# Kernel optimization log

Hardware: AMD Instinct MI355X
Metric: run time of the kernel (lower is better)

Reference implementation:

```python
import jax, jax.numpy as jnp
import numpy as np

N = 16384      # points
C = 512        # channels (d_model)
D_INNER = 1024 # expand=2
D_STATE = 16
D_CONV = 4
DT_RANK = 32   # ceil(C/16)
MLP = 1024     # mlp_ratio=2
EPS = 1e-5


def setup_inputs() -> dict:
    key = jax.random.key(0)
    ks = jax.random.split(key, 16)
    s = 0.02
    feat = jax.random.normal(ks[0], (N, C), jnp.float32)
    perm = np.random.RandomState(0).permutation(N)
    order = jnp.asarray(perm, jnp.int32)
    inverse = jnp.asarray(np.argsort(perm), jnp.int32)
    inp = dict(
        feat=feat, order=order, inverse=inverse,
        ln1_w=jnp.ones((C,)), ln1_b=jnp.zeros((C,)),
        in_proj_w=s * jax.random.normal(ks[1], (2 * D_INNER, C)),
        conv_w=s * jax.random.normal(ks[2], (D_INNER, D_CONV)),
        conv_b=jnp.zeros((D_INNER,)),
        x_proj_w=s * jax.random.normal(ks[3], (DT_RANK + 2 * D_STATE, D_INNER)),
        dt_proj_w=s * jax.random.normal(ks[4], (D_INNER, DT_RANK)),
        dt_proj_b=jnp.full((D_INNER,), -2.0),  # softplus(-2) ~ small dt, like mamba init
        A_log=jnp.log(jnp.tile(jnp.arange(1, D_STATE + 1, dtype=jnp.float32)[None, :], (D_INNER, 1))),
        D_skip=jnp.ones((D_INNER,)),
        out_proj_w=s * jax.random.normal(ks[5], (C, D_INNER)),
        ln2_w=jnp.ones((C,)), ln2_b=jnp.zeros((C,)),
        ffn_w1=s * jax.random.normal(ks[6], (C, MLP)), ffn_b1=jnp.zeros((MLP,)),
        ffn_w2=s * jax.random.normal(ks[7], (MLP, C)), ffn_b2=jnp.zeros((C,)),
    )
    return inp


def _layer_norm(x, w, b):
    mu = jnp.mean(x, axis=-1, keepdims=True)
    var = jnp.mean(jnp.square(x - mu), axis=-1, keepdims=True)
    return (x - mu) * jax.lax.rsqrt(var + EPS) * w + b


def _mamba(x, in_proj_w, conv_w, conv_b, x_proj_w, dt_proj_w, dt_proj_b,
           A_log, D_skip, out_proj_w):
    # x: (L, C)
    L = x.shape[0]
    xz = x @ in_proj_w.T                      # (L, 2*D_INNER)
    xm, z = jnp.split(xz, 2, axis=-1)
    # depthwise causal conv1d, kernel D_CONV
    xp = jnp.pad(xm, ((D_CONV - 1, 0), (0, 0)))
    xc = conv_b + sum(xp[k:k + L] * conv_w[:, k] for k in range(D_CONV))
    xc = jax.nn.silu(xc)                      # (L, D_INNER)
    dbc = xc @ x_proj_w.T                     # (L, DT_RANK + 2*D_STATE)
    dt, Bm, Cm = jnp.split(dbc, [DT_RANK, DT_RANK + D_STATE], axis=-1)
    dt = jax.nn.softplus(dt @ dt_proj_w.T + dt_proj_b)  # (L, D_INNER)
    A = -jnp.exp(A_log)                       # (D_INNER, D_STATE)

    def step(h, inp):
        dt_t, B_t, C_t, x_t = inp             # (D_INNER,), (D_STATE,), (D_STATE,), (D_INNER,)
        dA = jnp.exp(dt_t[:, None] * A)       # (D_INNER, D_STATE)
        h = dA * h + (dt_t * x_t)[:, None] * B_t[None, :]
        return h, h @ C_t                     # y_t: (D_INNER,)

    h0 = jnp.zeros((D_INNER, D_STATE), xm.dtype)
    _, ys = jax.lax.scan(step, h0, (dt, Bm, Cm, xc))
    y = (ys + xc * D_skip) * jax.nn.silu(z)
    return y @ out_proj_w.T                   # (L, C)


def reference(feat, order, inverse, ln1_w, ln1_b, in_proj_w, conv_w, conv_b,
              x_proj_w, dt_proj_w, dt_proj_b, A_log, D_skip, out_proj_w,
              ln2_w, ln2_b, ffn_w1, ffn_b1, ffn_w2, ffn_b2):
    f = feat[order]                           # gather by serialized order
    x = f + _mamba(_layer_norm(f, ln1_w, ln1_b), in_proj_w, conv_w, conv_b,
                   x_proj_w, dt_proj_w, dt_proj_b, A_log, D_skip, out_proj_w)
    h = _layer_norm(x, ln2_w, ln2_b)
    x = x + (jax.nn.gelu(h @ ffn_w1 + ffn_b1, approximate=False) @ ffn_w2 + ffn_b2)
    return x[inverse]                         # scatter back to original order
```

## Files before the change

kernel.cpp:

```cpp
#include <hip/hip_runtime.h>


#define DEV __device__ __forceinline__

typedef unsigned short u16;
typedef u16    u16x8  __attribute__((ext_vector_type(8)));
typedef __bf16 bf16x8 __attribute__((ext_vector_type(8)));
typedef float  f32x4  __attribute__((ext_vector_type(4)));

static constexpr int L_SEQ = 16384;
static constexpr int LC    = 64;
static constexpr int NCH   = 256;

DEV u16 f2b(float x){
  union { float f; unsigned u; } c; c.f = x;
  unsigned u = c.u;
  return (u16)((u + 0x7fffu + ((u >> 16) & 1u)) >> 16);
}
DEV float b2f(u16 h){
  union { unsigned u; float f; } c; c.u = ((unsigned)h) << 16;
  return c.f;
}
DEV int ldix(const void* p, int l, bool is64){
  return is64 ? (int)((const long long*)p)[l] : ((const int*)p)[l];
}
DEV float siluf(float x){ return x / (1.f + __expf(-x)); }
DEV float softplusf(float x){
  return fmaxf(x, 0.f) + __logf(1.f + __expf(-fabsf(x)));
}
DEV float geluf(float x){ return 0.5f * x * (1.f + erff(x * 0.70710678118f)); }

DEV void gld_lds16(const u16* g, u16* l){
  __builtin_amdgcn_global_load_lds(
      (const __attribute__((address_space(1))) unsigned*)g,
      (__attribute__((address_space(3))) unsigned*)l, 16, 0, 0);
}

DEV void pow16(float r, float* a){
  float r2 = r * r, r4 = r2 * r2, r8 = r4 * r4;
  a[0] = r;        a[1] = r2;       a[2] = r2 * r;    a[3] = r4;
  a[4] = r4 * r;   a[5] = r4 * r2;  a[6] = r4 * a[2]; a[7] = r8;
  a[8] = r8 * r;   a[9] = r8 * r2;  a[10] = r8 * a[2]; a[11] = r8 * r4;
  a[12] = r8 * a[4]; a[13] = r8 * a[5]; a[14] = r8 * a[6]; a[15] = r8 * r8;
}

__global__ __launch_bounds__(256) void fill_k(float* out, float v, unsigned n){
  unsigned i = blockIdx.x * 256 + threadIdx.x;
  if (i < n) out[i] = v;
}

__global__ void detect_k(const int* ord32, int* flag){
  flag[0] = (ord32[1] == 0 && ord32[3] == 0 && ord32[5] == 0) ? 1 : 0;
  flag[1] = 0;
}

__global__ __launch_bounds__(256) void checkA_k(const float* __restrict__ alog,
                                                int* flag){
  int i = blockIdx.x * 256 + threadIdx.x;
  int s = i & 15;
  float v = alog[i];
  float base = alog[i - s];
  if (fabsf(v - (base + __logf((float)(s + 1)))) > 1e-4f) atomicOr(flag + 1, 1);
}

struct NT4 { const float* src[4]; unsigned off[5]; };
__global__ __launch_bounds__(256) void normw_k(NT4 t, u16* dst){
  unsigned i = blockIdx.x * 256 + threadIdx.x;
  if (i >= t.off[4]) return;
  int s = 0;
  #pragma unroll
  for (int k = 1; k <= 3; k++) s += (i >= t.off[k]) ? 1 : 0;
  dst[i] = f2b(t.src[s][i - t.off[s]]);
}

__global__ __launch_bounds__(256) void convT_kernel(const float* __restrict__ in,
                                                    u16* __restrict__ out, int K, int N){
  __shared__ float t[32][33];
  int k0 = blockIdx.x * 32, n0 = blockIdx.y * 32;
  int tx = threadIdx.x & 31, ty = threadIdx.x >> 5;
  #pragma unroll
  for (int i = 0; i < 32; i += 8)
    t[ty + i][tx] = in[(size_t)(k0 + ty + i) * N + n0 + tx];
  __syncthreads();
  #pragma unroll
  for (int i = 0; i < 32; i += 8)
    out[(size_t)(n0 + ty + i) * K + k0 + tx] = f2b(t[tx][ty + i]);
}

__global__ __launch_bounds__(256) void gather_ln1(const float* __restrict__ feat,
    const void* order, const float* __restrict__ w, const float* __restrict__ b,
    const int* flag, u16* __restrict__ x1b){
  __shared__ float rs_[256], rq_[256];
  const bool is64 = flag[0] != 0;
  int l = blockIdx.x, tid = threadIdx.x;
  int src = ldix(order, l, is64);
  float v0 = feat[(size_t)src * 512 + tid];
  float v1 = feat[(size_t)src * 512 + tid + 256];
  rs_[tid] = v0 + v1; rq_[tid] = v0 * v0 + v1 * v1;
  __syncthreads();
  for (int o = 128; o; o >>= 1){
    if (tid < o){ rs_[tid] += rs_[tid + o]; rq_[tid] += rq_[tid + o]; }
    __syncthreads();
  }
  float mu = rs_[0] * (1.f / 512.f);
  float var = rq_[0] * (1.f / 512.f) - mu * mu;
  float rstd = rsqrtf(var + 1e-5f);
  x1b[(size_t)l * 512 + tid]       = f2b((v0 - mu) * rstd * w[tid]       + b[tid]);
  x1b[(size_t)l * 512 + tid + 256] = f2b((v1 - mu) * rstd * w[tid + 256] + b[tid + 256]);
}

__global__ __launch_bounds__(256) void ln2_kernel(const float* __restrict__ x,
    const float* __restrict__ w, const float* __restrict__ b, u16* __restrict__ h2b){
  __shared__ float rs_[256], rq_[256];
  int l = blockIdx.x, tid = threadIdx.x;
  float v0 = x[(size_t)l * 512 + tid];
  float v1 = x[(size_t)l * 512 + tid + 256];
  rs_[tid] = v0 + v1; rq_[tid] = v0 * v0 + v1 * v1;
  __syncthreads();
  for (int o = 128; o; o >>= 1){
    if (tid < o){ rs_[tid] += rs_[tid + o]; rq_[tid] += rq_[tid + o]; }
    __syncthreads();
  }
  float mu = rs_[0] * (1.f / 512.f);
  float var = rq_[0] * (1.f / 512.f) - mu * mu;
  float rstd = rsqrtf(var + 1e-5f);
  h2b[(size_t)l * 512 + tid]       = f2b((v0 - mu) * rstd * w[tid]       + b[tid]);
  h2b[(size_t)l * 512 + tid + 256] = f2b((v1 - mu) * rstd * w[tid + 256] + b[tid + 256]);
}

__global__ __launch_bounds__(256) void conv_silu(const u16* __restrict__ xm,
    const float* __restrict__ cw, const float* __restrict__ cb, u16* __restrict__ xcb){
  constexpr int TT = 8;
  const int tid = threadIdx.x;
  const int d0 = (tid & 127) * 8;
  const int t0 = (blockIdx.x * 2 + (tid >> 7)) * TT;

  float wk[4][8], bias[8];
  #pragma unroll
  for (int j = 0; j < 8; j++) bias[j] = cb[d0 + j];
  #pragma unroll
  for (int j = 0; j < 8; j++){
    f32x4 v = *(const f32x4*)(cw + (d0 + j) * 4);
    wk[0][j] = v[0]; wk[1][j] = v[1]; wk[2][j] = v[2]; wk[3][j] = v[3];
  }

  float win[3][8];
  #pragma unroll
  for (int k = 0; k < 3; k++){
    int tt = t0 - 3 + k;
    if (tt >= 0){
      u16x8 v = *(const u16x8*)(xm + (size_t)tt * 1024 + d0);
      #pragma unroll
      for (int j = 0; j < 8; j++) win[k][j] = b2f(v[j]);
    } else {
      #pragma unroll
      for (int j = 0; j < 8; j++) win[k][j] = 0.f;
    }
  }

  #pragma unroll
  for (int t = 0; t < TT; t++){
    u16x8 v = *(const u16x8*)(xm + (size_t)(t0 + t) * 1024 + d0);
    u16x8 o;
    float cu[8];
    #pragma unroll
    for (int j = 0; j < 8; j++){
      cu[j] = b2f(v[j]);
      float acc = bias[j] + win[0][j] * wk[0][j] + win[1][j] * wk[1][j]
                + win[2][j] * wk[2][j] + cu[j] * wk[3][j];
      o[j] = f2b(siluf(acc));
    }
    *(u16x8*)(xcb + (size_t)(t0 + t) * 1024 + d0) = o;
    #pragma unroll
    for (int j = 0; j < 8; j++){
      win[0][j] = win[1][j]; win[1][j] = win[2][j]; win[2][j] = cu[j];
    }
  }
}

enum { M_BF16 = 0, M_INPROJ = 1, M_DT = 2, M_RES = 3, M_GELU = 4, M_FFN2 = 5 };

template<int MODE>
DEV void gemm_epilogue(float v, int m, int n, int N,
    float* __restrict__ outf, u16* __restrict__ outb, u16* __restrict__ outb2,
    const float* __restrict__ auxf, const float* __restrict__ auxw,
    const void* ordv, bool is64){
  size_t o = (size_t)m * N + n;
  if constexpr (MODE == M_BF16){
    outb[o] = f2b(v);
  } else if constexpr (MODE == M_INPROJ){
    if (n < 1024) outb [(size_t)m * 1024 + n]          = f2b(v);
    else          outb2[(size_t)m * 1024 + (n - 1024)] = f2b(siluf(v));
  } else if constexpr (MODE == M_DT){
    outb[o] = f2b(softplusf(v + auxw[n]));
  } else if constexpr (MODE == M_RES){
    int src = ldix(ordv, m, is64);
    outf[o] = v + auxw[(size_t)src * 512 + n];
  } else if constexpr (MODE == M_GELU){
    outb[o] = f2b(geluf(v + auxw[n]));
  } else {
    outf[o] = v + auxw[n] + auxf[o];
  }
}

#define PH8(BUF, MH, KS, LOADB, ...)                                        \
  do {                                                                      \
    bf16x8 af_[4];                                                          \
    _Pragma("unroll")                                                       \
    for (int mi = 0; mi < 4; mi++){                                         \
      int R = wr * 128 + (MH) * 64 + mi * 16 + rr;                          \
      int slot = ((KS) * 4 + qc) ^ (R & 7);                                 \
      af_[mi] = *(const bf16x8*)(&sA[BUF][R * 64 + slot * 8]);              \
    }                                                                       \
    if constexpr (LOADB){                                                   \
      _Pragma("unroll")                                                     \
      for (int nj = 0; nj < 4; nj++){                                       \
        int R = wc * 64 + nj * 16 + rr;                                     \
        int slot = ((KS) * 4 + qc) ^ (R & 7);                               \
        bfr[KS][nj] = *(const bf16x8*)(&sB[BUF][R * 64 + slot * 8]);        \
      }                                                                     \
    }                                                                       \
    __VA_ARGS__;                                                            \
    __builtin_amdgcn_s_barrier();                                           \
    asm volatile("s_waitcnt lgkmcnt(0)" ::: "memory");                      \
    __builtin_amdgcn_sched_barrier(0);                                      \
    __builtin_amdgcn_s_setprio(1);                                          \
    _Pragma("unroll")                                                       \
    for (int mi = 0; mi < 4; mi++)                                          \
      _Pragma("unroll")                                                     \
      for (int nj = 0; nj < 4; nj++)                                        \
        acc[(MH) * 4 + mi][nj] = __builtin_amdgcn_mfma_f32_16x16x32_bf16(   \
            af_[mi], bfr[KS][nj], acc[(MH) * 4 + mi][nj], 0, 0, 0);         \
    __builtin_amdgcn_s_setprio(0);                                          \
    __builtin_amdgcn_s_barrier();                                           \
  } while (0)

template<int MODE>
__global__ __launch_bounds__(512, 2) void gemm_8ph(
    const u16* __restrict__ A, const u16* __restrict__ B,
    int N, int K, int lda, int ldb,
    float* __restrict__ outf, u16* __restrict__ outb, u16* __restrict__ outb2,
    const float* __restrict__ auxf, const float* __restrict__ auxw,
    const void* ordv, const int* flag){
  __shared__ __align__(16) u16 sA[2][256 * 64];
  __shared__ __align__(16) u16 sB[2][256 * 64];
  const int tid  = threadIdx.x;
  const int wave = tid >> 6, lane = tid & 63;
  const int wr = wave >> 2, wc = wave & 3;
  const int m0 = blockIdx.x * 256, n0 = blockIdx.y * 256;
  const int rr = lane & 15, qc = lane >> 4;

  f32x4  acc[8][4] = {};
  bf16x8 bfr[2][4];

  const int srow = tid >> 3, ssub = tid & 7;
  auto stA = [&](int buf, int band, int kt){
    int row = band * 64 + srow;
    int cg = ssub ^ (row & 7);
    gld_lds16(A + (size_t)(m0 + row) * lda + kt * 64 + cg * 8,
              &sA[buf][band * 4096 + tid * 8]);
  };
  auto stB = [&](int buf, int band, int kt){
    int row = band * 64 + srow;
    int cg = ssub ^ (row & 7);
    gld_lds16(B + (size_t)(n0 + row) * ldb + kt * 64 + cg * 8,
              &sB[buf][band * 4096 + tid * 8]);
  };

  const int nst = K / 64, its = nst / 2;

  stA(0,0,0); stA(0,1,0); stA(0,2,0); stA(0,3,0);
  stB(0,0,0); stB(0,1,0); stB(0,2,0); stB(0,3,0);
  stB(1,0,1); stB(1,1,1); stB(1,2,1); stB(1,3,1);
  stA(1,0,1); stA(1,2,1);
  asm volatile("s_waitcnt vmcnt(6)" ::: "memory");
  __builtin_amdgcn_s_barrier();

  for (int it = 0; it < its; ++it){
    const int k2  = 2 * it + 1;
    const int kn1 = 2 * it + 2, kn2 = 2 * it + 3;
    const bool pre = (it + 1 < its);
    PH8(0, 0, 0, true,  stA(1,1,k2); stA(1,3,k2) );
    PH8(0, 0, 1, true,  ((void)0) );
    PH8(0, 1, 0, false, if (pre){ stB(0,0,kn1); stB(0,1,kn1); } );
    PH8(0, 1, 1, false,
        if (pre){ stB(0,2,kn1); stB(0,3,kn1); stA(0,0,kn1);
                  asm volatile("s_waitcnt vmcnt(5)" ::: "memory"); }
        else    { asm volatile("s_waitcnt vmcnt(0)" ::: "memory"); } );
    PH8(1, 0, 0, true,  if (pre){ stA(0,2,kn1); stA(0,1,kn1); stA(0,3,kn1); } );
    PH8(1, 0, 1, true,  ((void)0) );
    PH8(1, 1, 0, false, if (pre){ stB(1,0,kn2); stB(1,1,kn2); stB(1,2,kn2); } );
    PH8(1, 1, 1, false,
        if (pre){ stB(1,3,kn2); stA(1,0,kn2); stA(1,2,kn2);
                  asm volatile("s_waitcnt vmcnt(6)" ::: "memory"); } );
  }

  const bool is64 = flag ? (flag[0] != 0) : false;
  #pragma unroll
  for (int mi = 0; mi < 8; mi++)
    #pragma unroll
    for (int nj = 0; nj < 4; nj++)
      #pragma unroll
      for (int r = 0; r < 4; r++){
        int m = m0 + wr * 128 + mi * 16 + ((lane >> 4) << 2) + r;
        int n = n0 + wc * 64 + nj * 16 + (lane & 15);
        gemm_epilogue<MODE>(acc[mi][nj][r], m, n, N, outf, outb, outb2,
                            auxf, auxw, ordv, is64);
      }
}

template<int BM, int BN, int WM, int WN, int MODE>
__global__ __launch_bounds__((BM / WM) * (BN / WN) * 64) void gemm_p2(
    const u16* __restrict__ A, const u16* __restrict__ B,
    int N, int K, int lda, int ldb,
    float* __restrict__ outf, u16* __restrict__ outb, u16* __restrict__ outb2,
    const float* __restrict__ auxf, const float* __restrict__ auxw,
    const void* ordv, const int* flag){
  constexpr int BK = 32;
  constexpr int MI = WM / 16, NI = WN / 16;
  constexpr int WCOLS = BN / WN;
  constexpr int THREADS = (BM / WM) * (BN / WN) * 64;
  constexpr int NA = BM * BK / (THREADS * 8);
  constexpr int NB = BN * BK / (THREADS * 8);
  constexpr int LPS = NA + NB;
  static_assert(LPS == 2 || LPS == 3 || LPS == 4, "vmcnt literals");
  __shared__ __align__(16) u16 sA[3][BM * BK];
  __shared__ __align__(16) u16 sB[3][BN * BK];
  const int tid  = threadIdx.x;
  const int wave = tid >> 6, lane = tid & 63;
  const int wr = wave / WCOLS, wc = wave % WCOLS;
  const int m0 = blockIdx.x * BM, n0 = blockIdx.y * BN;
  const int rr = lane & 15;
  const int qc = lane >> 4;

  f32x4 acc[MI][NI] = {};

  auto stage = [&](int buf, int k0){
    #pragma unroll
    for (int i = 0; i < NA; i++){
      int idx = tid + i * THREADS;
      int row = idx >> 2, sub = idx & 3;
      int cg = (sub - (row >> 1)) & 3;
      gld_lds16(A + (size_t)(m0 + row) * lda + k0 + cg * 8, &sA[buf][idx * 8]);
    }
    #pragma unroll
    for (int i = 0; i < NB; i++){
      int idx = tid + i * THREADS;
      int row = idx >> 2, sub = idx & 3;
      int cg = (sub - (row >> 1)) & 3;
      gld_lds16(B + (size_t)(n0 + row) * ldb + k0 + cg * 8, &sB[buf][idx * 8]);
    }
  };

  const int nst = K / BK;
  stage(0, 0);
  if (nst > 1) stage(1, BK);
  for (int st = 0; st < nst; st++){
    if (st + 2 < nst) stage((st + 2) % 3, (st + 2) * BK);
    const int nf = (st + 2 < nst) ? 2 : ((st + 1 < nst) ? 1 : 0);
    if (nf == 2){
      if constexpr (LPS == 4)      asm volatile("s_waitcnt vmcnt(8)" ::: "memory");
      else if constexpr (LPS == 3) asm volatile("s_waitcnt vmcnt(6)" ::: "memory");
      else                         asm volatile("s_waitcnt vmcnt(4)" ::: "memory");
    } else if (nf == 1){
      if constexpr (LPS == 4)      asm volatile("s_waitcnt vmcnt(4)" ::: "memory");
      else if constexpr (LPS == 3) asm volatile("s_waitcnt vmcnt(3)" ::: "memory");
      else                         asm volatile("s_waitcnt vmcnt(2)" ::: "memory");
    } else {
      asm volatile("s_waitcnt vmcnt(0)" ::: "memory");
    }
    __builtin_amdgcn_s_barrier();
    __builtin_amdgcn_sched_barrier(0);

    const int cur = st % 3;
    bf16x8 af[MI], bfr[NI];
    #pragma unroll
    for (int i = 0; i < MI; i++){
      int R = wr * WM + i * 16 + rr;
      int slot = (qc + (R >> 1)) & 3;
      af[i] = *(const bf16x8*)(&sA[cur][R * BK + slot * 8]);
    }
    #pragma unroll
    for (int j = 0; j < NI; j++){
      int R = wc * WN + j * 16 + rr;
      int slot = (qc + (R >> 1)) & 3;
      bfr[j] = *(const bf16x8*)(&sB[cur][R * BK + slot * 8]);
    }
    #pragma unroll
    for (int i = 0; i < MI; i++)
      #pragma unroll
      for (int j = 0; j < NI; j++)
        acc[i][j] = __builtin_amdgcn_mfma_f32_16x16x32_bf16(af[i], bfr[j], acc[i][j], 0, 0, 0);

    asm volatile("s_waitcnt lgkmcnt(0)" ::: "memory");
    __builtin_amdgcn_s_barrier();
    __builtin_amdgcn_sched_barrier(0);
  }

  const bool is64 = flag ? (flag[0] != 0) : false;
  #pragma unroll
  for (int i = 0; i < MI; i++)
    #pragma unroll
    for (int j = 0; j < NI; j++)
      #pragma unroll
      for (int r = 0; r < 4; r++){
        int m = m0 + wr * WM + i * 16 + ((lane >> 4) << 2) + r;
        int n = n0 + wc * WN + j * 16 + (lane & 15);
        gemm_epilogue<MODE>(acc[i][j][r], m, n, N, outf, outb, outb2,
                            auxf, auxw, ordv, is64);
      }
}

template<int BM, int BN, int WM, int WN, int MODE>
__global__ __launch_bounds__(256) void gemm_bt(
    const u16* __restrict__ A, const u16* __restrict__ B,
    int N, int K, int lda, int ldb,
    float* __restrict__ outf, u16* __restrict__ outb, u16* __restrict__ outb2,
    const float* __restrict__ auxf, const float* __restrict__ auxw,
    const void* ordv, const int* flag){
  constexpr int BK = 32;
  constexpr int MI = WM / 16, NI = WN / 16;
  constexpr int WCOLS = BN / WN;
  constexpr int NA = BM * 4 / 256;
  constexpr int NB = BN * 4 / 256;
  __shared__ __align__(16) u16 sA[BM * BK];
  __shared__ __align__(16) u16 sB[BN * BK];
  const int tid  = threadIdx.x;
  const int wave = tid >> 6, lane = tid & 63;
  const int wr = wave / WCOLS, wc = wave % WCOLS;
  const int m0 = blockIdx.x * BM, n0 = blockIdx.y * BN;
  const int rr = lane & 15;
  const int qk = (lane >> 4) * 8;

  f32x4 acc[MI][NI] = {};

  for (int k0 = 0; k0 < K; k0 += BK){
    #pragma unroll
    for (int i = 0; i < NA; i++){
      int idx = tid + i * 256;
      int r = idx >> 2, c = (idx & 3) * 8;
      gld_lds16(A + (size_t)(m0 + r) * lda + k0 + c, sA + (size_t)idx * 8);
    }
    #pragma unroll
    for (int i = 0; i < NB; i++){
      int idx = tid + i * 256;
      int r = idx >> 2, c = (idx & 3) * 8;
      gld_lds16(B + (size_t)(n0 + r) * ldb + k0 + c, sB + (size_t)idx * 8);
    }
    __syncthreads();

    bf16x8 af[MI], bfr[NI];
    #pragma unroll
    for (int i = 0; i < MI; i++)
      af[i] = *(const bf16x8*)(sA + (wr * WM + i * 16 + rr) * BK + qk);
    #pragma unroll
    for (int j = 0; j < NI; j++)
      bfr[j] = *(const bf16x8*)(sB + (wc * WN + j * 16 + rr) * BK + qk);
    #pragma unroll
    for (int i = 0; i < MI; i++)
      #pragma unroll
      for (int j = 0; j < NI; j++)
        acc[i][j] = __builtin_amdgcn_mfma_f32_16x16x32_bf16(af[i], bfr[j], acc[i][j], 0, 0, 0);
    __syncthreads();
  }

  const bool is64 = flag ? (flag[0] != 0) : false;
  #pragma unroll
  for (int i = 0; i < MI; i++)
    #pragma unroll
    for (int j = 0; j < NI; j++)
      #pragma unroll
      for (int r = 0; r < 4; r++){
        int m = m0 + wr * WM + i * 16 + ((lane >> 4) << 2) + r;
        int n = n0 + wc * WN + j * 16 + (lane & 15);
        gemm_epilogue<MODE>(acc[i][j][r], m, n, N, outf, outb, outb2,
                            auxf, auxw, ordv, is64);
      }
}

__global__ __launch_bounds__(256) void scan_pass1(const u16* __restrict__ dt,
    const u16* __restrict__ xc, const u16* __restrict__ dbc,
    const float* __restrict__ alog, const int* __restrict__ flag,
    u16* __restrict__ chP, u16* __restrict__ chH){
  __shared__ float sB[LC * 16];
  const int chunk = blockIdx.x;
  const int d = blockIdx.y * 256 + threadIdx.x;
  const int t0 = chunk * LC;
  for (int i = threadIdx.x; i < LC * 16; i += 256){
    int t = i >> 4, s = i & 15;
    sB[i] = b2f(dbc[(size_t)(t0 + t) * 64 + 32 + s]);
  }
  __syncthreads();
  float h[16];
  #pragma unroll
  for (int s = 0; s < 16; s++) h[s] = 0.f;
  float P[16];
  const bool fastA = (flag[1] == 0);
  if (fastA){
    const float a0 = -__expf(alog[(size_t)d * 16]);
    float R = 1.f;
    for (int t = 0; t < LC; t++){
      float dtv = b2f(dt[(size_t)(t0 + t) * 1024 + d]);
      float xv  = b2f(xc[(size_t)(t0 + t) * 1024 + d]);
      float dtx = dtv * xv;
      float r = __expf(dtv * a0);
      R *= r;
      float a_[16];
      pow16(r, a_);
      #pragma unroll
      for (int s = 0; s < 16; s++)
        h[s] = a_[s] * h[s] + dtx * sB[t * 16 + s];
    }
    pow16(R, P);
  } else {
    float A[16];
    #pragma unroll
    for (int s = 0; s < 16; s++){
      A[s] = -__expf(alog[(size_t)d * 16 + s]);
      P[s] = 1.f;
    }
    for (int t = 0; t < LC; t++){
      float dtv = b2f(dt[(size_t)(t0 + t) * 1024 + d]);
      float xv  = b2f(xc[(size_t)(t0 + t) * 1024 + d]);
      float dtx = dtv * xv;
      #pragma unroll
      for (int s = 0; s < 16; s++){
        float a = __expf(dtv * A[s]);
        P[s] *= a;
        h[s] = a * h[s] + dtx * sB[t * 16 + s];
      }
    }
  }
  #pragma unroll
  for (int s = 0; s < 16; s++){
    chP[((size_t)chunk * 16 + s) * 1024 + d] = f2b(P[s]);
    chH[((size_t)chunk * 16 + s) * 1024 + d] = f2b(h[s]);
  }
}

__global__ __launch_bounds__(64) void carry_scan(const u16* chP, const u16* chH,
                                                 u16* hin){
  int id = blockIdx.x * 64 + threadIdx.x;
  float h = 0.f;
  for (int k = 0; k < NCH; k += 8){
    float P[8], E[8];
    #pragma unroll
    for (int j = 0; j < 8; j++){
      P[j] = b2f(chP[(size_t)(k + j) * 16384 + id]);
      E[j] = b2f(chH[(size_t)(k + j) * 16384 + id]);
    }
    #pragma unroll
    for (int j = 0; j < 8; j++){
      hin[(size_t)(k + j) * 16384 + id] = f2b(h);
      h = P[j] * h + E[j];
    }
  }
}

__global__ __launch_bounds__(256) void scan_pass3(const u16* __restrict__ dt,
    const u16* xc, const u16* __restrict__ dbc,
    const float* __restrict__ alog, const int* __restrict__ flag,
    const u16* __restrict__ hin,
    const float* __restrict__ dskip, const u16* __restrict__ zsil, u16* yb){
  __shared__ float sBC[LC * 32];
  const int chunk = blockIdx.x;
  const int d = blockIdx.y * 256 + threadIdx.x;
  const int t0 = chunk * LC;
  for (int i = threadIdx.x; i < LC * 32; i += 256){
    int t = i >> 5, c = i & 31;
    sBC[i] = b2f(dbc[(size_t)(t0 + t) * 64 + 32 + c]);
  }
  __syncthreads();
  float h[16];
  #pragma unroll
  for (int s = 0; s < 16; s++)
    h[s] = b2f(hin[((size_t)chunk * 16 + s) * 1024 + d]);
  const float Dv = dskip[d];
  const bool fastA = (flag[1] == 0);
  if (fastA){
    const float a0 = -__expf(alog[(size_t)d * 16]);
    for (int t = 0; t < LC; t++){
      float dtv = b2f(dt[(size_t)(t0 + t) * 1024 + d]);
      float xv  = b2f(xc[(size_t)(t0 + t) * 1024 + d]);
      float dtx = dtv * xv;
      float r = __expf(dtv * a0);
      float a_[16];
      pow16(r, a_);
      float y = 0.f;
      #pragma unroll
      for (int s = 0; s < 16; s++){
        h[s] = a_[s] * h[s] + dtx * sBC[t * 32 + s];
        y += h[s] * sBC[t * 32 + 16 + s];
      }
      float rv = (y + xv * Dv) * b2f(zsil[(size_t)(t0 + t) * 1024 + d]);
      yb[(size_t)(t0 + t) * 1024 + d] = f2b(rv);
    }
  } else {
    float A[16];
    #pragma unroll
    for (int s = 0; s < 16; s++) A[s] = -__expf(alog[(size_t)d * 16 + s]);
    for (int t = 0; t < LC; t++){
      float dtv = b2f(dt[(size_t)(t0 + t) * 1024 + d]);
      float xv  = b2f(xc[(size_t)(t0 + t) * 1024 + d]);
      float dtx = dtv * xv;
      float y = 0.f;
      #pragma unroll
      for (int s = 0; s < 16; s++){
        float a = __expf(dtv * A[s]);
        h[s] = a * h[s] + dtx * sBC[t * 32 + s];
        y += h[s] * sBC[t * 32 + 16 + s];
      }
      float rv = (y + xv * Dv) * b2f(zsil[(size_t)(t0 + t) * 1024 + d]);
      yb[(size_t)(t0 + t) * 1024 + d] = f2b(rv);
    }
  }
}

__global__ __launch_bounds__(256) void final_gather(const float* __restrict__ xfin,
    const void* inv, const int* flag, float* __restrict__ out){
  const bool is64 = flag[0] != 0;
  int i = blockIdx.x, tid = threadIdx.x;
  int src = ldix(inv, i, is64);
  out[(size_t)i * 512 + tid]       = xfin[(size_t)src * 512 + tid];
  out[(size_t)i * 512 + tid + 256] = xfin[(size_t)src * 512 + tid + 256];
}

extern "C" void kernel_launch(void* const* d_in, const int* in_sizes, int n_in,
                              void* d_out, int out_size, void* d_ws, size_t ws_size,
                              hipStream_t stream){
  float* out = (float*)d_out;
  char* w = (char*)d_ws;

  constexpr size_t OFF_W1T  = 3342336;
  constexpr size_t OFF_W2T  = OFF_W1T + 1048576;
  constexpr size_t OFF_FLAG = OFF_W2T + 1048576;
  constexpr size_t OFF_XMB  = 5439744;
  constexpr size_t OFF_ZSIL = OFF_XMB  + 33554432;
  constexpr size_t OFF_XCB  = OFF_ZSIL + 33554432;
  constexpr size_t OFF_X1B  = OFF_XCB  + 33554432;
  constexpr size_t OFF_DBC  = OFF_X1B  + 16777216;
  constexpr size_t OFF_CHP  = OFF_X1B;
  constexpr size_t OFF_CHH  = OFF_X1B  + 8388608;
  constexpr size_t WS_NEED  = OFF_DBC  + 2097152;

  int code = 0;
  static const int want[20] = {8388608,16384,16384,512,512,1048576,4096,1024,
                               65536,32768,1024,16384,1024,524288,512,512,
                               524288,1024,524288,512};
  if (n_in != 20) code = 1000;
  else {
    for (int i = 0; i < 20 && !code; i++)
      if (in_sizes[i] != want[i]) code = 2000 + i * 50;
    if (!code && out_size != 8388608) code = 3000;
    if (!code && ws_size < WS_NEED)   code = 4000;
  }
  if (code){
    unsigned n = (unsigned)(out_size > 0 ? out_size : 1);
    fill_k<<<(n + 255) / 256, 256, 0, stream>>>(out, (float)code, n);
    return;
  }

  u16*   w1tb = (u16*)(w + OFF_W1T);
  u16*   w2tb = (u16*)(w + OFF_W2T);
  int*   flag = (int*)(w + OFF_FLAG);
  u16*   xmb  = (u16*)(w + OFF_XMB);
  u16*   zsil = (u16*)(w + OFF_ZSIL);
  u16*   xcb  = (u16*)(w + OFF_XCB);
  u16*   x1b  = (u16*)(w + OFF_X1B);
  u16*   dbcb = (u16*)(w + OFF_DBC);
  u16*   chP  = (u16*)(w + OFF_CHP);
  u16*   chH  = (u16*)(w + OFF_CHH);
  float* x    = (float*)(w + OFF_XMB);
  float* xfin = (float*)(w + OFF_XCB);
  u16* dtb  = xmb;
  u16* yb   = xcb;
  u16* midb = zsil;
  u16* h2b  = x1b;
  u16* hin  = chP;

  u16* nb = (u16*)w;
  u16* inpjn  = nb;
  u16* xpjn   = nb + 1048576;
  u16* dtpjn  = nb + 1114112;
  u16* outpjn = nb + 1146880;
  NT4 t;
  t.src[0] = (const float*)d_in[5];  t.src[1] = (const float*)d_in[8];
  t.src[2] = (const float*)d_in[9];  t.src[3] = (const float*)d_in[13];
  t.off[0] = 0; t.off[1] = 1048576; t.off[2] = 1114112; t.off[3] = 1146880; t.off[4] = 1671168;

  detect_k<<<1, 1, 0, stream>>>((const int*)d_in[1], flag);
  checkA_k<<<64, 256, 0, stream>>>((const float*)d_in[11], flag);
  normw_k<<<(1671168 + 255) / 256, 256, 0, stream>>>(t, nb);
  convT_kernel<<<dim3(16, 32), 256, 0, stream>>>((const float*)d_in[16], w1tb, 512, 1024);
  convT_kernel<<<dim3(32, 16), 256, 0, stream>>>((const float*)d_in[18], w2tb, 1024, 512);

  gather_ln1<<<L_SEQ, 256, 0, stream>>>((const float*)d_in[0], d_in[1],
      (const float*)d_in[3], (const float*)d_in[4], flag, x1b);

  gemm_8ph<M_INPROJ><<<dim3(64,8),512,0,stream>>>(
      x1b, inpjn, 2048, 512, 512, 512, nullptr, xmb, zsil, nullptr, nullptr, nullptr, nullptr);

  conv_silu<<<1024, 256, 0, stream>>>(xmb,
      (const float*)d_in[6], (const float*)d_in[7], xcb);

  gemm_p2<64,64,16,64,M_BF16><<<dim3(256,1),256,0,stream>>>(
      xcb, xpjn, 64, 1024, 1024, 1024, nullptr, dbcb, nullptr, nullptr, nullptr, nullptr, nullptr);

  gemm_bt<128,128,64,64,M_DT><<<dim3(128,8),256,0,stream>>>(
      dbcb, dtpjn, 1024, 32, 64, 32, nullptr, dtb, nullptr, nullptr,
      (const float*)d_in[10], nullptr, nullptr);

  scan_pass1<<<dim3(NCH,4),256,0,stream>>>(dtb, xcb, dbcb,
      (const float*)d_in[11], flag, chP, chH);
  carry_scan<<<256,64,0,stream>>>(chP, chH, hin);
  scan_pass3<<<dim3(NCH,4),256,0,stream>>>(dtb, xcb, dbcb,
      (const float*)d_in[11], flag, hin, (const float*)d_in[12], zsil, yb);

  gemm_p2<256,128,64,64,M_RES><<<dim3(64,4),512,0,stream>>>(
      yb, outpjn, 512, 1024, 1024, 1024, x, nullptr, nullptr, nullptr,
      (const float*)d_in[0], d_in[1], flag);

  ln2_kernel<<<L_SEQ,256,0,stream>>>(x, (const float*)d_in[14], (const float*)d_in[15], h2b);

  gemm_8ph<M_GELU><<<dim3(64,4),512,0,stream>>>(
      h2b, w1tb, 1024, 512, 512, 512, nullptr, midb, nullptr, nullptr,
      (const float*)d_in[17], nullptr, nullptr);

  gemm_p2<256,128,64,64,M_FFN2><<<dim3(64,4),512,0,stream>>>(
      midb, w2tb, 512, 1024, 1024, 1024, xfin, nullptr, nullptr, x,
      (const float*)d_in[19], nullptr, nullptr);

  final_gather<<<L_SEQ,256,0,stream>>>(xfin, d_in[2], flag, out);
}
```

Measured before the change: 504.5 us.

## Fuse prep kernels, scatter FFN2 output directly, vectorize layernorms

Merges the checkA, weight-normalization and two transpose kernels into one prep launch to cut launch overhead. The final FFN2 GEMM epilogue now scatters each row straight to its original position using the order index, which removes the separate final_gather kernel and its 32MB round trip. The two layernorm kernels switch to float2 loads and packed bf16 stores. The carry scan also unrolls 16 chunks instead of 8. The scattered epilogue writes rows non-contiguously, which may cost some store efficiency.

```diff
diff --git a/kernel.cpp b/kernel.cpp
--- a/kernel.cpp
+++ b/kernel.cpp
@@ -54,37 +54,38 @@
   flag[1] = 0;
 }
 
-__global__ __launch_bounds__(256) void checkA_k(const float* __restrict__ alog,
-                                                int* flag){
-  int i = blockIdx.x * 256 + threadIdx.x;
-  int s = i & 15;
-  float v = alog[i];
-  float base = alog[i - s];
-  if (fabsf(v - (base + __logf((float)(s + 1)))) > 1e-4f) atomicOr(flag + 1, 1);
-}
-
 struct NT4 { const float* src[4]; unsigned off[5]; };
-__global__ __launch_bounds__(256) void normw_k(NT4 t, u16* dst){
-  unsigned i = blockIdx.x * 256 + threadIdx.x;
-  if (i >= t.off[4]) return;
-  int s = 0;
-  #pragma unroll
-  for (int k = 1; k <= 3; k++) s += (i >= t.off[k]) ? 1 : 0;
-  dst[i] = f2b(t.src[s][i - t.off[s]]);
-}
-
-__global__ __launch_bounds__(256) void convT_kernel(const float* __restrict__ in,
-                                                    u16* __restrict__ out, int K, int N){
-  __shared__ float t[32][33];
-  int k0 = blockIdx.x * 32, n0 = blockIdx.y * 32;
-  int tx = threadIdx.x & 31, ty = threadIdx.x >> 5;
-  #pragma unroll
-  for (int i = 0; i < 32; i += 8)
-    t[ty + i][tx] = in[(size_t)(k0 + ty + i) * N + n0 + tx];
-  __syncthreads();
-  #pragma unroll
-  for (int i = 0; i < 32; i += 8)
-    out[(size_t)(n0 + ty + i) * K + k0 + tx] = f2b(t[tx][ty + i]);
+__global__ __launch_bounds__(256) void prep_k(NT4 t, u16* dst,
+    const float* w1in, u16* w1tb, const float* w2in, u16* w2tb,
+    const float* alog, int* flag){
+  __shared__ float ts[32][33];
+  const int b = blockIdx.x;
+  if (b < 6528){
+    unsigned i = (unsigned)b * 256 + threadIdx.x;
+    int s = 0;
+    #pragma unroll
+    for (int k = 1; k <= 3; k++) s += (i >= t.off[k]) ? 1 : 0;
+    dst[i] = f2b(t.src[s][i - t.off[s]]);
+  } else if (b < 7552){
+    const float* in; u16* outp; int K, N, bx, by;
+    if (b < 7040){ int id = b - 6528; in = w1in; outp = w1tb; K = 512;  N = 1024; bx = id & 15; by = id >> 4; }
+    else         { int id = b - 7040; in = w2in; outp = w2tb; K = 1024; N = 512;  bx = id & 31; by = id >> 5; }
+    int k0 = bx * 32, n0 = by * 32;
+    int tx = threadIdx.x & 31, ty = threadIdx.x >> 5;
+    #pragma unroll
+    for (int i = 0; i < 32; i += 8)
+      ts[ty + i][tx] = in[(size_t)(k0 + ty + i) * N + n0 + tx];
+    __syncthreads();
+    #pragma unroll
+    for (int i = 0; i < 32; i += 8)
+      outp[(size_t)(n0 + ty + i) * K + k0 + tx] = f2b(ts[tx][ty + i]);
+  } else {
+    int i = (b - 7552) * 256 + threadIdx.x;
+    int s = i & 15;
+    float v = alog[i];
+    float base = alog[i - s];
+    if (fabsf(v - (base + __logf((float)(s + 1)))) > 1e-4f) atomicOr(flag + 1, 1);
+  }
 }
 
 __global__ __launch_bounds__(256) void gather_ln1(const float* __restrict__ feat,
@@ -94,9 +95,8 @@
   const bool is64 = flag[0] != 0;
   int l = blockIdx.x, tid = threadIdx.x;
   int src = ldix(order, l, is64);
-  float v0 = feat[(size_t)src * 512 + tid];
-  float v1 = feat[(size_t)src * 512 + tid + 256];
-  rs_[tid] = v0 + v1; rq_[tid] = v0 * v0 + v1 * v1;
+  float2 v = *(const float2*)(feat + (size_t)src * 512 + 2 * tid);
+  rs_[tid] = v.x + v.y; rq_[tid] = v.x * v.x + v.y * v.y;
   __syncthreads();
   for (int o = 128; o; o >>= 1){
     if (tid < o){ rs_[tid] += rs_[tid + o]; rq_[tid] += rq_[tid + o]; }
@@ -105,17 +105,19 @@
   float mu = rs_[0] * (1.f / 512.f);
   float var = rq_[0] * (1.f / 512.f) - mu * mu;
   float rstd = rsqrtf(var + 1e-5f);
-  x1b[(size_t)l * 512 + tid]       = f2b((v0 - mu) * rstd * w[tid]       + b[tid]);
-  x1b[(size_t)l * 512 + tid + 256] = f2b((v1 - mu) * rstd * w[tid + 256] + b[tid + 256]);
+  float2 wv = *(const float2*)(w + 2 * tid);
+  float2 bv = *(const float2*)(b + 2 * tid);
+  unsigned pack = (unsigned)f2b((v.x - mu) * rstd * wv.x + bv.x)
+                | ((unsigned)f2b((v.y - mu) * rstd * wv.y + bv.y) << 16);
+  *(unsigned*)(x1b + (size_t)l * 512 + 2 * tid) = pack;
 }
 
 __global__ __launch_bounds__(256) void ln2_kernel(const float* __restrict__ x,
     const float* __restrict__ w, const float* __restrict__ b, u16* __restrict__ h2b){
   __shared__ float rs_[256], rq_[256];
   int l = blockIdx.x, tid = threadIdx.x;
-  float v0 = x[(size_t)l * 512 + tid];
-  float v1 = x[(size_t)l * 512 + tid + 256];
-  rs_[tid] = v0 + v1; rq_[tid] = v0 * v0 + v1 * v1;
+  float2 v = *(const float2*)(x + (size_t)l * 512 + 2 * tid);
+  rs_[tid] = v.x + v.y; rq_[tid] = v.x * v.x + v.y * v.y;
   __syncthreads();
   for (int o = 128; o; o >>= 1){
     if (tid < o){ rs_[tid] += rs_[tid + o]; rq_[tid] += rq_[tid + o]; }
@@ -124,8 +126,11 @@
   float mu = rs_[0] * (1.f / 512.f);
   float var = rq_[0] * (1.f / 512.f) - mu * mu;
   float rstd = rsqrtf(var + 1e-5f);
-  h2b[(size_t)l * 512 + tid]       = f2b((v0 - mu) * rstd * w[tid]       + b[tid]);
-  h2b[(size_t)l * 512 + tid + 256] = f2b((v1 - mu) * rstd * w[tid + 256] + b[tid + 256]);
+  float2 wv = *(const float2*)(w + 2 * tid);
+  float2 bv = *(const float2*)(b + 2 * tid);
+  unsigned pack = (unsigned)f2b((v.x - mu) * rstd * wv.x + bv.x)
+                | ((unsigned)f2b((v.y - mu) * rstd * wv.y + bv.y) << 16);
+  *(unsigned*)(h2b + (size_t)l * 512 + 2 * tid) = pack;
 }
 
 __global__ __launch_bounds__(256) void conv_silu(const u16* __restrict__ xm,
@@ -178,7 +183,7 @@
   }
 }
 
-enum { M_BF16 = 0, M_INPROJ = 1, M_DT = 2, M_RES = 3, M_GELU = 4, M_FFN2 = 5 };
+enum { M_BF16 = 0, M_INPROJ = 1, M_DT = 2, M_RES = 3, M_GELU = 4, M_FFN2S = 5 };
 
 template<int MODE>
 DEV void gemm_epilogue(float v, int m, int n, int N,
@@ -199,7 +204,8 @@
   } else if constexpr (MODE == M_GELU){
     outb[o] = f2b(geluf(v + auxw[n]));
   } else {
-    outf[o] = v + auxw[n] + auxf[o];
+    int dst = ldix(ordv, m, is64);
+    outf[(size_t)dst * 512 + n] = v + auxw[n] + auxf[o];
   }
 }
 
@@ -542,15 +548,15 @@
                                                  u16* hin){
   int id = blockIdx.x * 64 + threadIdx.x;
   float h = 0.f;
-  for (int k = 0; k < NCH; k += 8){
-    float P[8], E[8];
-    #pragma unroll
-    for (int j = 0; j < 8; j++){
+  for (int k = 0; k < NCH; k += 16){
+    float P[16], E[16];
+    #pragma unroll
+    for (int j = 0; j < 16; j++){
       P[j] = b2f(chP[(size_t)(k + j) * 16384 + id]);
       E[j] = b2f(chH[(size_t)(k + j) * 16384 + id]);
     }
     #pragma unroll
-    for (int j = 0; j < 8; j++){
+    for (int j = 0; j < 16; j++){
       hin[(size_t)(k + j) * 16384 + id] = f2b(h);
       h = P[j] * h + E[j];
     }
@@ -616,15 +622,6 @@
   }
 }
 
-__global__ __launch_bounds__(256) void final_gather(const float* __restrict__ xfin,
-    const void* inv, const int* flag, float* __restrict__ out){
-  const bool is64 = flag[0] != 0;
-  int i = blockIdx.x, tid = threadIdx.x;
-  int src = ldix(inv, i, is64);
-  out[(size_t)i * 512 + tid]       = xfin[(size_t)src * 512 + tid];
-  out[(size_t)i * 512 + tid + 256] = xfin[(size_t)src * 512 + tid + 256];
-}
-
 extern "C" void kernel_launch(void* const* d_in, const int* in_sizes, int n_in,
                               void* d_out, int out_size, void* d_ws, size_t ws_size,
                               hipStream_t stream){
@@ -671,7 +668,6 @@
   u16*   chP  = (u16*)(w + OFF_CHP);
   u16*   chH  = (u16*)(w + OFF_CHH);
   float* x    = (float*)(w + OFF_XMB);
-  float* xfin = (float*)(w + OFF_XCB);
   u16* dtb  = xmb;
   u16* yb   = xcb;
   u16* midb = zsil;
@@ -689,10 +685,9 @@
   t.off[0] = 0; t.off[1] = 1048576; t.off[2] = 1114112; t.off[3] = 1146880; t.off[4] = 1671168;
 
   detect_k<<<1, 1, 0, stream>>>((const int*)d_in[1], flag);
-  checkA_k<<<64, 256, 0, stream>>>((const float*)d_in[11], flag);
-  normw_k<<<(1671168 + 255) / 256, 256, 0, stream>>>(t, nb);
-  convT_kernel<<<dim3(16, 32), 256, 0, stream>>>((const float*)d_in[16], w1tb, 512, 1024);
-  convT_kernel<<<dim3(32, 16), 256, 0, stream>>>((const float*)d_in[18], w2tb, 1024, 512);
+  prep_k<<<7616, 256, 0, stream>>>(t, nb,
+      (const float*)d_in[16], w1tb, (const float*)d_in[18], w2tb,
+      (const float*)d_in[11], flag);
 
   gather_ln1<<<L_SEQ, 256, 0, stream>>>((const float*)d_in[0], d_in[1],
       (const float*)d_in[3], (const float*)d_in[4], flag, x1b);
@@ -726,9 +721,7 @@
       h2b, w1tb, 1024, 512, 512, 512, nullptr, midb, nullptr, nullptr,
       (const float*)d_in[17], nullptr, nullptr);
 
-  gemm_p2<256,128,64,64,M_FFN2><<<dim3(64,4),512,0,stream>>>(
-      midb, w2tb, 512, 1024, 1024, 1024, xfin, nullptr, nullptr, x,
-      (const float*)d_in[19], nullptr, nullptr);
-
-  final_gather<<<L_SEQ,256,0,stream>>>(xfin, d_in[2], flag, out);
-}
+  gemm_p2<256,128,64,64,M_FFN2S><<<dim3(64,4),512,0,stream>>>(
+      midb, w2tb, 512, 1024, 1024, 1024, out, nullptr, nullptr, x,
+      (const float*)d_in[19], d_in[1], flag);
+}
```

New measurement: 491.2 us. -2.6%, faster.
